# Performance work log

Hardware: AMD Instinct MI355X
Metric: run time of the kernel (lower is better)

## Reference

```python
import jax, jax.numpy as jnp
import numpy as np

B, N, D = 256, 256, 256
DELTA_BEARING = 5.0
DELTA_HEADING = 5.0
N_HEAD = int(360 / DELTA_HEADING)   # 72
N_BEAR = int(360 / DELTA_BEARING)   # 72
DOMAIN_PARAM = 2.0
EPS = 1e-14


def setup_inputs() -> dict:
    key = jax.random.key(0)
    ks = jax.random.split(key, 8)
    hidden_state = jax.random.normal(ks[0], (B, N, D), dtype=jnp.float32)
    distance_matrix = jax.random.uniform(ks[1], (B, N, N), dtype=jnp.float32) * 10.0
    bearing_matrix = jax.random.uniform(ks[2], (B, N, N), dtype=jnp.float32) * 360.0
    heading_matrix = jax.random.uniform(ks[3], (B, N, N), dtype=jnp.float32) * 360.0
    sequence_mask = (jax.random.uniform(ks[4], (B, N)) > 0.1).astype(jnp.float32)
    domain = jnp.full((N_HEAD, N_BEAR), DOMAIN_PARAM, dtype=jnp.float32)
    lim = 1.0 / np.sqrt(2 * D)
    W = jax.random.uniform(ks[5], (D, 2 * D), minval=-lim, maxval=lim, dtype=jnp.float32)
    b = jax.random.uniform(ks[6], (D,), minval=-lim, maxval=lim, dtype=jnp.float32)
    return {"hidden_state": hidden_state, "distance_matrix": distance_matrix,
            "bearing_matrix": bearing_matrix, "heading_matrix": heading_matrix,
            "sequence_mask": sequence_mask, "domain": domain, "W": W, "b": b}


def _compute_weights(domain, distance_matrix, bearing_matrix, heading_matrix, sequence_mask):
    # domain lookup indices from heading/bearing bins
    idx1 = jnp.clip(jnp.floor((heading_matrix + DELTA_HEADING / 2) / DELTA_HEADING), 0, N_HEAD - 1).astype(jnp.int32)
    idx2 = jnp.clip(jnp.floor((bearing_matrix + DELTA_BEARING / 2) / DELTA_BEARING), 0, N_BEAR - 1).astype(jnp.int32)
    w = jax.nn.relu(domain[idx1, idx2] - distance_matrix)  # (B,N,N)
    # pairwise sequence mask and no-self-attention mask
    wm = sequence_mask[:, :, None] * sequence_mask[:, None, :]  # (B,N,N)
    ped = 1.0 - jnp.eye(w.shape[1], dtype=w.dtype)               # (N,N)
    valid = (ped[None, :, :] * wm) > 0
    w = jnp.where(valid, w, 0.0)
    # masked softmax over dim=2: zeros are treated as masked, epsilon-stabilized
    mask = (w != 0).astype(w.dtype)
    masked_exps = jnp.exp(w) * mask + EPS
    w = masked_exps / (masked_exps.sum(axis=2, keepdims=True) + EPS)
    return jnp.where(valid, w, 0.0)


def reference(hidden_state, distance_matrix, bearing_matrix, heading_matrix, sequence_mask, domain, W, b):
    weights = _compute_weights(domain, distance_matrix, bearing_matrix, heading_matrix, sequence_mask)
    weighted_hidden = jnp.einsum('bij,bjd->bid', weights, hidden_state)  # (B,N,D)
    cat = jnp.concatenate([weighted_hidden, hidden_state], axis=-1)       # (B,N,2D)
    return jnp.einsum('bnk,dk->bnd', cat, W) + b
```

## Files before the change

kernel.cpp:

```cpp
#include <hip/hip_runtime.h>
#include <hip/hip_bf16.h>


typedef __attribute__((ext_vector_type(4))) float  f32x4;
typedef __attribute__((ext_vector_type(8))) short  bf16x8;
typedef __attribute__((ext_vector_type(4))) short  bf16x4;

#define EPSC 1e-14f

__device__ __forceinline__ short f2bf(float v) {
  __hip_bfloat16 h = __float2bfloat16(v);
  return *reinterpret_cast<short*>(&h);
}
__device__ __forceinline__ void gload16(const void* g, void* l) {
  __builtin_amdgcn_global_load_lds(
      (const __attribute__((address_space(1))) void*)g,
      (__attribute__((address_space(3))) void*)l, 16, 0, 0);
}
__device__ __forceinline__ bf16x8 cvt8(const float* p) {
  f32x4 a = *(const f32x4*)p;
  f32x4 b = *(const f32x4*)(p + 4);
  bf16x8 r;
  r[0] = f2bf(a[0]); r[1] = f2bf(a[1]); r[2] = f2bf(a[2]); r[3] = f2bf(a[3]);
  r[4] = f2bf(b[0]); r[5] = f2bf(b[1]); r[6] = f2bf(b[2]); r[7] = f2bf(b[3]);
  return r;
}

__global__ void k0_pack(const float* __restrict__ W, short* __restrict__ Wbf) {
  int idx = blockIdx.x * 256 + threadIdx.x;
  f32x4 v = *(const f32x4*)(W + (size_t)idx * 4);
  bf16x4 pk;
  pk[0] = f2bf(v[0]); pk[1] = f2bf(v[1]); pk[2] = f2bf(v[2]); pk[3] = f2bf(v[3]);
  *(bf16x4*)(Wbf + (size_t)idx * 4) = pk;
}

__global__ void k0_check(const float* __restrict__ domain, float* __restrict__ flag) {
  __shared__ int s_ok[4];
  const int t = threadIdx.x;
  float v0 = domain[0];
  bool ok = true;
  for (int x = t; x < 72 * 72; x += 256) ok = ok && (domain[x] == v0);
  unsigned long long m = __ballot(ok);
  if ((t & 63) == 0) s_ok[t >> 6] = (m == ~0ull) ? 1 : 0;
  __syncthreads();
  if (t == 0) {
    flag[0] = v0;
    flag[1] = (s_ok[0] && s_ok[1] && s_ok[2] && s_ok[3]) ? 1.f : 0.f;
  }
}

__global__ __launch_bounds__(256) void k2a_weights(
    const float* __restrict__ dist, const float* __restrict__ bear,
    const float* __restrict__ head, const float* __restrict__ seqmask,
    const float* __restrict__ domain, const float* __restrict__ uflag,
    short* __restrict__ weBuf) {
  __shared__ float sMask[256];
  const int t = threadIdx.x;
  const int b = blockIdx.x >> 3;
  const int i0 = (blockIdx.x & 7) * 32;
  if (t < 256) sMask[t] = seqmask[b * 256 + t];
  __syncthreads();

  const int w = t >> 6, l = t & 63;
  const int j0 = l * 4;
  const float dval = uflag[0];
  const bool  uni  = uflag[1] != 0.f;
  const f32x4 mj = *(const f32x4*)(sMask + j0);

  f32x4 dv[8];
  #pragma unroll
  for (int rr = 0; rr < 8; ++rr) {
    int i = i0 + w * 8 + rr;
    dv[rr] = *(const f32x4*)(dist + ((size_t)b * 256 + i) * 256 + j0);
  }

  #pragma unroll
  for (int rr = 0; rr < 8; ++rr) {
    const int i = i0 + w * 8 + rr;
    const float mI = sMask[i];
    const size_t base = ((size_t)b * 256 + i) * 256;
    float ev[4];
    float rs = 0.f;
    if (uni) {
      #pragma unroll
      for (int e = 0; e < 4; ++e) {
        float wv = fmaxf(dval - dv[rr][e], 0.f);
        bool valid = (i != j0 + e) && (mI != 0.f) && (mj[e] != 0.f);
        float ex = (wv > 0.f) ? __expf(wv) : 0.f;
        ex = valid ? ex : 0.f;
        rs += ex;
        ev[e] = valid ? (ex + EPSC) : 0.f;
      }
    } else {
      f32x4 bv = *(const f32x4*)(bear + base + j0);
      f32x4 hv = *(const f32x4*)(head + base + j0);
      #pragma unroll
      for (int e = 0; e < 4; ++e) {
        float f1 = fminf(fmaxf(floorf((hv[e] + 2.5f) * 0.2f), 0.f), 71.f);
        float f2 = fminf(fmaxf(floorf((bv[e] + 2.5f) * 0.2f), 0.f), 71.f);
        float wv = fmaxf(domain[(int)(f1 * 72.f + f2)] - dv[rr][e], 0.f);
        bool valid = (i != j0 + e) && (mI != 0.f) && (mj[e] != 0.f);
        float ex = (wv > 0.f) ? __expf(wv) : 0.f;
        ex = valid ? ex : 0.f;
        rs += ex;
        ev[e] = valid ? (ex + EPSC) : 0.f;
      }
    }
    rs += __shfl_xor(rs, 1, 64);
    rs += __shfl_xor(rs, 2, 64);
    rs += __shfl_xor(rs, 4, 64);
    rs += __shfl_xor(rs, 8, 64);
    rs += __shfl_xor(rs, 16, 64);
    rs += __shfl_xor(rs, 32, 64);
    const float scale = 1.0f / (rs + 257.0f * EPSC);
    bf16x4 pk;
    pk[0] = f2bf(ev[0] * scale); pk[1] = f2bf(ev[1] * scale);
    pk[2] = f2bf(ev[2] * scale); pk[3] = f2bf(ev[3] * scale);
    *(bf16x4*)(weBuf + base + j0) = pk;
  }
}

__global__ __launch_bounds__(512, 4) void k1_p1t(
    const float* __restrict__ H, const short* __restrict__ Wbf,
    short* __restrict__ P1T) {
  extern __shared__ char sm[];
  char* sB0 = sm;
  char* sB1 = sm + 32768;
  const int t = threadIdx.x;
  const int x = blockIdx.x;
  const int blk = (x & 7) * 64 + (x >> 3);
  const int n0 = blk * 128;
  const int b  = n0 >> 8;
  const int jb = n0 & 255;

  const int wid = t >> 6, l = t & 63;
  const int lr = l & 15, lg = l >> 4;
  const int wr = wid & 3, wc = wid >> 2;
  const int r3 = l >> 3, sl = l & 7;
  const int sswz = (sl ^ r3) * 8;
  const int sw = (lr & 7) << 4;

  const size_t h0 = ((size_t)(n0 + wr * 32 + lr)) * 256;
  const size_t h1 = h0 + 16 * 256;

  #pragma unroll
  for (int p = 0; p < 4; ++p) {
    int dd = wid * 8 + r3 + 64 * p;
    gload16(Wbf + (size_t)dd * 512 + sswz, sB0 + (wid * 8 + 64 * p) * 128);
  }
  __syncthreads();

  f32x4 acc[2][8] = {};

  #pragma unroll
  for (int c = 0; c < 4; ++c) {
    char* cur = (c & 1) ? sB1 : sB0;
    char* nxt = (c & 1) ? sB0 : sB1;
    if (c < 3) {
      #pragma unroll
      for (int p = 0; p < 4; ++p) {
        int dd = wid * 8 + r3 + 64 * p;
        gload16(Wbf + (size_t)dd * 512 + (c + 1) * 64 + sswz, nxt + (wid * 8 + 64 * p) * 128);
      }
    }
    const int kk = c * 64;
    #pragma unroll
    for (int sub = 0; sub < 2; ++sub) {
      bf16x8 av0 = cvt8(H + h0 + kk + sub * 32 + lg * 8);
      bf16x8 av1 = cvt8(H + h1 + kk + sub * 32 + lg * 8);
      #pragma unroll
      for (int n = 0; n < 8; ++n) {
        const int d = wc * 128 + n * 16 + lr;
        bf16x8 bb = *(const bf16x8*)(cur + d * 128 + ((sub * 64 + lg * 16) ^ sw));
        acc[0][n] = __builtin_amdgcn_mfma_f32_16x16x32_bf16(av0, bb, acc[0][n], 0, 0, 0);
        acc[1][n] = __builtin_amdgcn_mfma_f32_16x16x32_bf16(av1, bb, acc[1][n], 0, 0, 0);
      }
    }
    __syncthreads();
  }

  #pragma unroll
  for (int m = 0; m < 2; ++m) {
    #pragma unroll
    for (int n = 0; n < 8; ++n) {
      const int d = wc * 128 + n * 16 + lr;
      f32x4 v = acc[m][n];
      bf16x4 pk;
      pk[0] = f2bf(v[0]); pk[1] = f2bf(v[1]); pk[2] = f2bf(v[2]); pk[3] = f2bf(v[3]);
      *(bf16x4*)(P1T + (size_t)b * 65536 + (size_t)d * 256 + jb + wr * 32 + m * 16 + lg * 4) = pk;
    }
  }
}

__global__ __launch_bounds__(512, 4) void k2b_gemm(
    const short* __restrict__ weBuf, const short* __restrict__ P1T,
    const short* __restrict__ Wbf, const float* __restrict__ H,
    const float* __restrict__ bias, float* __restrict__ out) {
  extern __shared__ char sm[];
  char*  sB0   = sm;
  char*  sB1   = sm + 32768;
  float* sBias = (float*)(sm + 65536);
  const int t = threadIdx.x;
  const int x = blockIdx.x;
  const int blk = (x & 7) * 64 + (x >> 3);
  const int b  = blk >> 1;
  const int i0 = (blk & 1) * 128;

  const int wid = t >> 6, l = t & 63;
  const int lr = l & 15, lg = l >> 4;
  const int wr = wid & 3, wc = wid >> 2;
  const int r3 = l >> 3, sl = l & 7;
  const int sswz = (sl ^ r3) * 8;
  const int sw = (lr & 7) << 4;

  const short* __restrict__ P1b = P1T + (size_t)b * 65536;
  const size_t a0 = ((size_t)b * 256 + i0 + wr * 32 + lr) * 256;
  const size_t a1 = a0 + 16 * 256;

  #pragma unroll
  for (int p = 0; p < 4; ++p) {
    int dd = wid * 8 + r3 + 64 * p;
    gload16(P1b + (size_t)dd * 256 + sswz, sB0 + (wid * 8 + 64 * p) * 128);
  }
  if (t < 256) sBias[t] = bias[t];
  __syncthreads();

  f32x4 acc[2][8] = {};

  #pragma unroll
  for (int g = 0; g < 8; ++g) {
    char* cur = (g & 1) ? sB1 : sB0;
    char* nxt = (g & 1) ? sB0 : sB1;
    if (g < 7) {
      const int nk = ((g + 1) & 3) * 64;
      if (g + 1 < 4) {
        #pragma unroll
        for (int p = 0; p < 4; ++p) {
          int dd = wid * 8 + r3 + 64 * p;
          gload16(P1b + (size_t)dd * 256 + nk + sswz, nxt + (wid * 8 + 64 * p) * 128);
        }
      } else {
        #pragma unroll
        for (int p = 0; p < 4; ++p) {
          int dd = wid * 8 + r3 + 64 * p;
          gload16(Wbf + (size_t)dd * 512 + 256 + nk + sswz, nxt + (wid * 8 + 64 * p) * 128);
        }
      }
    }
    const int kk = (g & 3) * 64;
    #pragma unroll
    for (int sub = 0; sub < 2; ++sub) {
      bf16x8 av0, av1;
      if (g < 4) {
        av0 = *(const bf16x8*)(weBuf + a0 + kk + sub * 32 + lg * 8);
        av1 = *(const bf16x8*)(weBuf + a1 + kk + sub * 32 + lg * 8);
      } else {
        av0 = cvt8(H + a0 + kk + sub * 32 + lg * 8);
        av1 = cvt8(H + a1 + kk + sub * 32 + lg * 8);
      }
      #pragma unroll
      for (int n = 0; n < 8; ++n) {
        const int d = wc * 128 + n * 16 + lr;
        bf16x8 bb = *(const bf16x8*)(cur + d * 128 + ((sub * 64 + lg * 16) ^ sw));
        acc[0][n] = __builtin_amdgcn_mfma_f32_16x16x32_bf16(av0, bb, acc[0][n], 0, 0, 0);
        acc[1][n] = __builtin_amdgcn_mfma_f32_16x16x32_bf16(av1, bb, acc[1][n], 0, 0, 0);
      }
    }
    __syncthreads();
  }

  #pragma unroll
  for (int m = 0; m < 2; ++m) {
    #pragma unroll
    for (int n = 0; n < 8; ++n) {
      const int d = wc * 128 + n * 16 + lr;
      const float bs = sBias[d];
      #pragma unroll
      for (int r = 0; r < 4; ++r) {
        const int row = i0 + wr * 32 + m * 16 + lg * 4 + r;
        out[((size_t)b * 256 + row) * 256 + d] = acc[m][n][r] + bs;
      }
    }
  }
}

extern "C" void kernel_launch(void* const* d_in, const int* in_sizes, int n_in,
                              void* d_out, int out_size, void* d_ws, size_t ws_size,
                              hipStream_t stream) {
  const float* hidden  = (const float*)d_in[0];
  const float* dist    = (const float*)d_in[1];
  const float* bear    = (const float*)d_in[2];
  const float* head    = (const float*)d_in[3];
  const float* seqmask = (const float*)d_in[4];
  const float* domain  = (const float*)d_in[5];
  const float* W       = (const float*)d_in[6];
  const float* bias    = (const float*)d_in[7];
  float* out = (float*)d_out;

  char* ws = (char*)d_ws;
  short* Wbf   = (short*)ws;
  float* flag  = (float*)(ws + 524288);
  short* P1T   = (short*)(ws + (1u << 20));
  short* weBuf = (short*)(ws + (1u << 20) + (32u << 20));

  k0_pack<<<128, 256, 0, stream>>>(W, Wbf);
  k0_check<<<1, 256, 0, stream>>>(domain, flag);
  k2a_weights<<<2048, 256, 0, stream>>>(dist, bear, head, seqmask, domain, flag, weBuf);
  k1_p1t<<<512, 512, 65536, stream>>>(hidden, Wbf, P1T);
  k2b_gemm<<<512, 512, 66560, stream>>>(weBuf, P1T, Wbf, hidden, bias, out);
}
```

Measured before the change: 107.5 us.

## Compute both hidden-state projections in one kernel and simplify output GEMM

The projection kernel now does both halves of W per batch in one 1024-thread block: H·W1 goes to P1T and H·W2+bias to a bf16 buffer P2. The output kernel then only multiplies the attention weights by P1T and adds P2, so hidden_state is no longer re-read and converted there. Both kernels now use 256 large blocks with 128KB of LDS, loaded in one shot instead of double-buffered. This costs occupancy and load/compute overlap, adds an extra bf16 rounding on the second projection, and adds a 32MB intermediate write and read.

```diff
diff --git a/kernel.cpp b/kernel.cpp
--- a/kernel.cpp
+++ b/kernel.cpp
@@ -11,6 +11,9 @@
 __device__ __forceinline__ short f2bf(float v) {
   __hip_bfloat16 h = __float2bfloat16(v);
   return *reinterpret_cast<short*>(&h);
+}
+__device__ __forceinline__ float bf2f(unsigned short u) {
+  union { unsigned int i; float f; } c; c.i = ((unsigned int)u) << 16; return c.f;
 }
 __device__ __forceinline__ void gload16(const void* g, void* l) {
   __builtin_amdgcn_global_load_lds(
@@ -120,22 +123,17 @@
   }
 }
 
-__global__ __launch_bounds__(512, 4) void k1_p1t(
+__global__ __launch_bounds__(1024) void kP(
     const float* __restrict__ H, const short* __restrict__ Wbf,
-    short* __restrict__ P1T) {
+    const float* __restrict__ bias,
+    short* __restrict__ P1T, short* __restrict__ P2) {
   extern __shared__ char sm[];
-  char* sB0 = sm;
-  char* sB1 = sm + 32768;
-  const int t = threadIdx.x;
-  const int x = blockIdx.x;
-  const int blk = (x & 7) * 64 + (x >> 3);
-  const int n0 = blk * 128;
-  const int b  = n0 >> 8;
-  const int jb = n0 & 255;
-
+  const int t = threadIdx.x;
+  const int b = blockIdx.x;
+  const int n0 = b * 256;
   const int wid = t >> 6, l = t & 63;
   const int lr = l & 15, lg = l >> 4;
-  const int wr = wid & 3, wc = wid >> 2;
+  const int wr = wid & 7, wc = wid >> 3;
   const int r3 = l >> 3, sl = l & 7;
   const int sswz = (sl ^ r3) * 8;
   const int sw = (lr & 7) << 4;
@@ -144,129 +142,112 @@
   const size_t h1 = h0 + 16 * 256;
 
   #pragma unroll
-  for (int p = 0; p < 4; ++p) {
-    int dd = wid * 8 + r3 + 64 * p;
-    gload16(Wbf + (size_t)dd * 512 + sswz, sB0 + (wid * 8 + 64 * p) * 128);
-  }
-  __syncthreads();
-
-  f32x4 acc[2][8] = {};
-
-  #pragma unroll
-  for (int c = 0; c < 4; ++c) {
-    char* cur = (c & 1) ? sB1 : sB0;
-    char* nxt = (c & 1) ? sB0 : sB1;
-    if (c < 3) {
-      #pragma unroll
-      for (int p = 0; p < 4; ++p) {
-        int dd = wid * 8 + r3 + 64 * p;
-        gload16(Wbf + (size_t)dd * 512 + (c + 1) * 64 + sswz, nxt + (wid * 8 + 64 * p) * 128);
-      }
-    }
-    const int kk = c * 64;
-    #pragma unroll
-    for (int sub = 0; sub < 2; ++sub) {
-      bf16x8 av0 = cvt8(H + h0 + kk + sub * 32 + lg * 8);
-      bf16x8 av1 = cvt8(H + h1 + kk + sub * 32 + lg * 8);
-      #pragma unroll
-      for (int n = 0; n < 8; ++n) {
-        const int d = wc * 128 + n * 16 + lr;
-        bf16x8 bb = *(const bf16x8*)(cur + d * 128 + ((sub * 64 + lg * 16) ^ sw));
-        acc[0][n] = __builtin_amdgcn_mfma_f32_16x16x32_bf16(av0, bb, acc[0][n], 0, 0, 0);
-        acc[1][n] = __builtin_amdgcn_mfma_f32_16x16x32_bf16(av1, bb, acc[1][n], 0, 0, 0);
+  for (int pass = 0; pass < 2; ++pass) {
+    #pragma unroll
+    for (int c = 0; c < 4; ++c) {
+      #pragma unroll
+      for (int p = 0; p < 2; ++p) {
+        int dd = wid * 8 + 128 * p + r3;
+        gload16(Wbf + (size_t)dd * 512 + pass * 256 + c * 64 + sswz,
+                sm + c * 32768 + (wid * 8 + 128 * p) * 128);
       }
     }
     __syncthreads();
-  }
-
-  #pragma unroll
-  for (int m = 0; m < 2; ++m) {
-    #pragma unroll
-    for (int n = 0; n < 8; ++n) {
-      const int d = wc * 128 + n * 16 + lr;
-      f32x4 v = acc[m][n];
-      bf16x4 pk;
-      pk[0] = f2bf(v[0]); pk[1] = f2bf(v[1]); pk[2] = f2bf(v[2]); pk[3] = f2bf(v[3]);
-      *(bf16x4*)(P1T + (size_t)b * 65536 + (size_t)d * 256 + jb + wr * 32 + m * 16 + lg * 4) = pk;
-    }
-  }
-}
-
-__global__ __launch_bounds__(512, 4) void k2b_gemm(
+
+    f32x4 acc[2][8] = {};
+    #pragma unroll
+    for (int c = 0; c < 4; ++c) {
+      #pragma unroll
+      for (int sub = 0; sub < 2; ++sub) {
+        const int k0 = c * 64 + sub * 32 + lg * 8;
+        bf16x8 av0 = cvt8(H + h0 + k0);
+        bf16x8 av1 = cvt8(H + h1 + k0);
+        #pragma unroll
+        for (int n = 0; n < 8; ++n) {
+          const int d = wc * 128 + n * 16 + lr;
+          bf16x8 bb = *(const bf16x8*)(sm + c * 32768 + d * 128 + ((sub * 64 + lg * 16) ^ sw));
+          acc[0][n] = __builtin_amdgcn_mfma_f32_16x16x32_bf16(av0, bb, acc[0][n], 0, 0, 0);
+          acc[1][n] = __builtin_amdgcn_mfma_f32_16x16x32_bf16(av1, bb, acc[1][n], 0, 0, 0);
+        }
+      }
+    }
+
+    if (pass == 0) {
+      #pragma unroll
+      for (int m = 0; m < 2; ++m) {
+        #pragma unroll
+        for (int n = 0; n < 8; ++n) {
+          const int d = wc * 128 + n * 16 + lr;
+          const int j = wr * 32 + m * 16 + lg * 4;
+          f32x4 v = acc[m][n];
+          bf16x4 pk;
+          pk[0] = f2bf(v[0]); pk[1] = f2bf(v[1]); pk[2] = f2bf(v[2]); pk[3] = f2bf(v[3]);
+          *(bf16x4*)(P1T + (size_t)b * 65536 + (size_t)d * 256 + j) = pk;
+        }
+      }
+    } else {
+      #pragma unroll
+      for (int m = 0; m < 2; ++m) {
+        #pragma unroll
+        for (int n = 0; n < 8; ++n) {
+          const int d = wc * 128 + n * 16 + lr;
+          const float bs = bias[d];
+          const int row = wr * 32 + m * 16 + lg * 4;
+          f32x4 v = acc[m][n];
+          #pragma unroll
+          for (int r = 0; r < 4; ++r)
+            P2[(size_t)b * 65536 + (size_t)(row + r) * 256 + d] = f2bf(v[r] + bs);
+        }
+      }
+    }
+    __syncthreads();
+  }
+}
+
+__global__ __launch_bounds__(1024) void kOut(
     const short* __restrict__ weBuf, const short* __restrict__ P1T,
-    const short* __restrict__ Wbf, const float* __restrict__ H,
-    const float* __restrict__ bias, float* __restrict__ out) {
+    const short* __restrict__ P2, float* __restrict__ out) {
   extern __shared__ char sm[];
-  char*  sB0   = sm;
-  char*  sB1   = sm + 32768;
-  float* sBias = (float*)(sm + 65536);
-  const int t = threadIdx.x;
-  const int x = blockIdx.x;
-  const int blk = (x & 7) * 64 + (x >> 3);
-  const int b  = blk >> 1;
-  const int i0 = (blk & 1) * 128;
-
+  const int t = threadIdx.x;
+  const int b = blockIdx.x;
   const int wid = t >> 6, l = t & 63;
   const int lr = l & 15, lg = l >> 4;
-  const int wr = wid & 3, wc = wid >> 2;
+  const int wr = wid & 7, wc = wid >> 3;
   const int r3 = l >> 3, sl = l & 7;
   const int sswz = (sl ^ r3) * 8;
   const int sw = (lr & 7) << 4;
 
   const short* __restrict__ P1b = P1T + (size_t)b * 65536;
-  const size_t a0 = ((size_t)b * 256 + i0 + wr * 32 + lr) * 256;
+  const size_t a0 = ((size_t)b * 256 + wr * 32 + lr) * 256;
   const size_t a1 = a0 + 16 * 256;
 
   #pragma unroll
-  for (int p = 0; p < 4; ++p) {
-    int dd = wid * 8 + r3 + 64 * p;
-    gload16(P1b + (size_t)dd * 256 + sswz, sB0 + (wid * 8 + 64 * p) * 128);
-  }
-  if (t < 256) sBias[t] = bias[t];
+  for (int c = 0; c < 4; ++c) {
+    #pragma unroll
+    for (int p = 0; p < 2; ++p) {
+      int dd = wid * 8 + 128 * p + r3;
+      gload16(P1b + (size_t)dd * 256 + c * 64 + sswz,
+              sm + c * 32768 + (wid * 8 + 128 * p) * 128);
+    }
+  }
   __syncthreads();
 
   f32x4 acc[2][8] = {};
-
-  #pragma unroll
-  for (int g = 0; g < 8; ++g) {
-    char* cur = (g & 1) ? sB1 : sB0;
-    char* nxt = (g & 1) ? sB0 : sB1;
-    if (g < 7) {
-      const int nk = ((g + 1) & 3) * 64;
-      if (g + 1 < 4) {
-        #pragma unroll
-        for (int p = 0; p < 4; ++p) {
-          int dd = wid * 8 + r3 + 64 * p;
-          gload16(P1b + (size_t)dd * 256 + nk + sswz, nxt + (wid * 8 + 64 * p) * 128);
-        }
-      } else {
-        #pragma unroll
-        for (int p = 0; p < 4; ++p) {
-          int dd = wid * 8 + r3 + 64 * p;
-          gload16(Wbf + (size_t)dd * 512 + 256 + nk + sswz, nxt + (wid * 8 + 64 * p) * 128);
-        }
-      }
-    }
-    const int kk = (g & 3) * 64;
+  #pragma unroll
+  for (int c = 0; c < 4; ++c) {
     #pragma unroll
     for (int sub = 0; sub < 2; ++sub) {
-      bf16x8 av0, av1;
-      if (g < 4) {
-        av0 = *(const bf16x8*)(weBuf + a0 + kk + sub * 32 + lg * 8);
-        av1 = *(const bf16x8*)(weBuf + a1 + kk + sub * 32 + lg * 8);
-      } else {
-        av0 = cvt8(H + a0 + kk + sub * 32 + lg * 8);
-        av1 = cvt8(H + a1 + kk + sub * 32 + lg * 8);
-      }
+      const int k0 = c * 64 + sub * 32 + lg * 8;
+      bf16x8 av0 = *(const bf16x8*)(weBuf + a0 + k0);
+      bf16x8 av1 = *(const bf16x8*)(weBuf + a1 + k0);
       #pragma unroll
       for (int n = 0; n < 8; ++n) {
         const int d = wc * 128 + n * 16 + lr;
-        bf16x8 bb = *(const bf16x8*)(cur + d * 128 + ((sub * 64 + lg * 16) ^ sw));
+        bf16x8 bb = *(const bf16x8*)(sm + c * 32768 + d * 128 + ((sub * 64 + lg * 16) ^ sw));
         acc[0][n] = __builtin_amdgcn_mfma_f32_16x16x32_bf16(av0, bb, acc[0][n], 0, 0, 0);
         acc[1][n] = __builtin_amdgcn_mfma_f32_16x16x32_bf16(av1, bb, acc[1][n], 0, 0, 0);
       }
     }
-    __syncthreads();
   }
 
   #pragma unroll
@@ -274,11 +255,11 @@
     #pragma unroll
     for (int n = 0; n < 8; ++n) {
       const int d = wc * 128 + n * 16 + lr;
-      const float bs = sBias[d];
+      const int row = wr * 32 + m * 16 + lg * 4;
       #pragma unroll
       for (int r = 0; r < 4; ++r) {
-        const int row = i0 + wr * 32 + m * 16 + lg * 4 + r;
-        out[((size_t)b * 256 + row) * 256 + d] = acc[m][n][r] + bs;
+        const size_t off = ((size_t)b * 256 + row + r) * 256 + d;
+        out[off] = acc[m][n][r] + bf2f((unsigned short)P2[off]);
       }
     }
   }
@@ -301,11 +282,12 @@
   short* Wbf   = (short*)ws;
   float* flag  = (float*)(ws + 524288);
   short* P1T   = (short*)(ws + (1u << 20));
-  short* weBuf = (short*)(ws + (1u << 20) + (32u << 20));
+  short* P2    = (short*)(ws + (1u << 20) + (32u << 20));
+  short* weBuf = (short*)(ws + (1u << 20) + (64u << 20));
 
   k0_pack<<<128, 256, 0, stream>>>(W, Wbf);
   k0_check<<<1, 256, 0, stream>>>(domain, flag);
   k2a_weights<<<2048, 256, 0, stream>>>(dist, bear, head, seqmask, domain, flag, weBuf);
-  k1_p1t<<<512, 512, 65536, stream>>>(hidden, Wbf, P1T);
-  k2b_gemm<<<512, 512, 66560, stream>>>(weBuf, P1T, Wbf, hidden, bias, out);
-}
+  kP<<<256, 1024, 131072, stream>>>(hidden, Wbf, bias, P1T, P2);
+  kOut<<<256, 1024, 131072, stream>>>(weBuf, P1T, P2, out);
+}
```

Result: slower. 173.7 us (+61.7%).
